# Kernel optimization log

Hardware: AMD Instinct MI355X
Metric: run time of the kernel (lower is better)

Reference implementation:

```python
import jax, jax.numpy as jnp
import numpy as np

S, L, B = 64, 64, 16
D_IN, D_ATTN = 1024, 512


def setup_inputs() -> dict:
    key = jax.random.key(0)
    ks = jax.random.split(key, 8)
    context = jax.random.normal(ks[0], (S, L, B, D_IN), dtype=jnp.float32)
    query = jax.random.normal(ks[1], (L, B, D_IN), dtype=jnp.float32)
    mask = jnp.ones((S, L, B), dtype=jnp.int32)
    # Linear params (torch layout: weight [out, in], bias [out])
    sc = 1.0 / np.sqrt(D_IN)
    Wc = jax.random.uniform(ks[2], (D_ATTN, D_IN), minval=-sc, maxval=sc, dtype=jnp.float32)
    bc = jax.random.uniform(ks[3], (D_ATTN,), minval=-sc, maxval=sc, dtype=jnp.float32)
    Wq = jax.random.uniform(ks[4], (D_ATTN, D_IN), minval=-sc, maxval=sc, dtype=jnp.float32)
    bq = jax.random.uniform(ks[5], (D_ATTN,), minval=-sc, maxval=sc, dtype=jnp.float32)
    v = jax.random.uniform(ks[6], (D_ATTN,), dtype=jnp.float32)  # torch.rand -> U[0,1)
    return {"context": context, "query": query, "mask": mask,
            "Wc": Wc, "bc": bc, "Wq": Wq, "bq": bq, "v": v}


def reference(context, query, mask, Wc, bc, Wq, bq, v):
    # context: [s,l,b,din], query: [l,b,din]
    context_proj = jnp.einsum('slbi,di->slbd', context, Wc) + bc  # [s,l,b,da]
    query_proj = jnp.einsum('lbi,di->lbd', query, Wq) + bq        # [l,b,da]
    scores = jnp.tanh(context_proj + query_proj[None])            # [s,l,b,da]
    scores = jnp.einsum('slbd,d->slb', scores, v)                 # [s,l,b]
    scores = jnp.where(mask == 0, jnp.float32(-1e9), scores)
    alpha = jax.nn.softmax(scores, axis=0)                        # softmax over s
    attn_output = jnp.einsum('slb,slbd->lbd', alpha, context)     # [l,b,din]
    return (attn_output, alpha)
```

## Files before the change

kernel.cpp:

```cpp
#include <hip/hip_runtime.h>
#include <hip/hip_fp16.h>
#include <stdint.h>

#define S_DIM 64
#define L_DIM 64
#define B_DIM 16
#define LB    1024
#define DIN   1024
#define DA    512
#define M_TOT 65536

using f16x8 = __attribute__((ext_vector_type(8))) _Float16;
using f32x4 = __attribute__((ext_vector_type(4))) float;

typedef const __attribute__((address_space(1))) void* gas_ptr;
typedef __attribute__((address_space(3))) void* las_ptr;

__device__ __forceinline__ void load_lds16(const void* g, void* l) {
    __builtin_amdgcn_global_load_lds((gas_ptr)g, (las_ptr)l, 16, 0, 0);
}

__device__ __forceinline__ float fast_tanh(float x) {
    return 1.0f - 2.0f / (__expf(2.0f * x) + 1.0f);
}

__global__ void cvt_all(const float* __restrict__ Wc, const float* __restrict__ Wq,
                        const float* __restrict__ q,
                        _Float16* __restrict__ Wch, _Float16* __restrict__ Wqh,
                        _Float16* __restrict__ Qh) {
    int i = blockIdx.x * 256 + threadIdx.x;
    if (i < DA * DIN)            Wch[i] = (_Float16)Wc[i];
    else if (i < 2 * DA * DIN)   Wqh[i - DA * DIN] = (_Float16)Wq[i - DA * DIN];
    else                         Qh[i - 2 * DA * DIN] = (_Float16)q[i - 2 * DA * DIN];
}

__global__ __launch_bounds__(256) void ctx_cvt(const float* __restrict__ src,
                                               _Float16* __restrict__ dst) {
    const size_t nchunk = (size_t)M_TOT * DIN / 8;
    size_t stride = (size_t)gridDim.x * 256;
    for (size_t c = (size_t)blockIdx.x * 256 + threadIdx.x; c < nchunk; c += stride) {
        f32x4 a = *(const f32x4*)(src + c * 8);
        f32x4 b = *(const f32x4*)(src + c * 8 + 4);
        f16x8 h = {(_Float16)a[0], (_Float16)a[1], (_Float16)a[2], (_Float16)a[3],
                   (_Float16)b[0], (_Float16)b[1], (_Float16)b[2], (_Float16)b[3]};
        *(f16x8*)(dst + c * 8) = h;
    }
}

__global__ __launch_bounds__(256) void qp_gemm(
    const _Float16* __restrict__ Qh,
    const _Float16* __restrict__ Wqh,
    const float* __restrict__ bq, const float* __restrict__ bc,
    float* __restrict__ qp)
{
    __shared__ __align__(16) _Float16 lA[64 * 64];
    __shared__ __align__(16) _Float16 lB[64 * 64];
    const int t = threadIdx.x;
    const int w = t >> 6, lane = t & 63;
    const int quad = lane >> 4, m16 = lane & 15;
    const int n0 = blockIdx.x * 64, lb0 = blockIdx.y * 64;

    f32x4 acc[4] = {};

    for (int kt = 0; kt < DIN / 64; ++kt) {
#pragma unroll
        for (int i = 0; i < 2; ++i) {
            int c = (w * 2 + i) * 64 + lane;
            int row = c >> 3;
            int kc = (c & 7) ^ (row & 7);
            load_lds16(Qh  + (size_t)(lb0 + row) * DIN + kt * 64 + kc * 8, (char*)lA + (size_t)c * 16);
            load_lds16(Wqh + (size_t)(n0  + row) * DIN + kt * 64 + kc * 8, (char*)lB + (size_t)c * 16);
        }
        __syncthreads();
#pragma unroll
        for (int kk = 0; kk < 64; kk += 32) {
            int cq = (kk >> 3) + quad;
            int ar = 16 * w + m16;
            f16x8 a = *(const f16x8*)((const char*)lA + ar * 128 + ((cq ^ (ar & 7)) * 16));
#pragma unroll
            for (int j = 0; j < 4; ++j) {
                int br = 16 * j + m16;
                f16x8 b = *(const f16x8*)((const char*)lB + br * 128 + ((cq ^ (br & 7)) * 16));
                acc[j] = __builtin_amdgcn_mfma_f32_16x16x32_f16(a, b, acc[j], 0, 0, 0);
            }
        }
        __syncthreads();
    }
#pragma unroll
    for (int j = 0; j < 4; ++j) {
        int n = n0 + 16 * j + m16;
        float bias = bq[n] + bc[n];
#pragma unroll
        for (int r = 0; r < 4; ++r) {
            int lb = lb0 + 16 * w + quad * 4 + r;
            qp[(size_t)lb * DA + n] = acc[j][r] + bias;
        }
    }
}

__global__ __launch_bounds__(256) void score_gemm2(
    const _Float16* __restrict__ ctxh,
    const _Float16* __restrict__ Wch,
    const float* __restrict__ qp,
    const float* __restrict__ v,
    float* __restrict__ scores)
{
    __shared__ __align__(16) _Float16 lA[128 * 64];
    __shared__ __align__(16) _Float16 lB[128 * 64];
    __shared__ float lP[2][128];

    const int t = threadIdx.x;
    const int w = t >> 6, lane = t & 63;
    const int quad = lane >> 4, m16 = lane & 15;
    const int wm = w & 1, wn = w >> 1;

    int bid = blockIdx.x;
    int xcd = bid & 7;
    int j2 = bid >> 3;
    int nq = j2 & 3;
    int mb = ((j2 >> 2) << 3) | xcd;
    const int m0 = mb * 128;
    const int n0 = nq * 128;

    f32x4 acc[4][4] = {};

    for (int kt = 0; kt < DIN / 64; ++kt) {
#pragma unroll
        for (int i = 0; i < 4; ++i) {
            int c = (w * 4 + i) * 64 + lane;
            int row = c >> 3;
            int kc = (c & 7) ^ (row & 7);
            load_lds16(ctxh + (size_t)(m0 + row) * DIN + kt * 64 + kc * 8,
                       (char*)lA + (size_t)c * 16);
            load_lds16(Wch  + (size_t)(n0 + row) * DIN + kt * 64 + kc * 8,
                       (char*)lB + (size_t)c * 16);
        }
        __syncthreads();
#pragma unroll
        for (int kk = 0; kk < 64; kk += 32) {
            int cq = (kk >> 3) + quad;
            f16x8 a[4], b[4];
#pragma unroll
            for (int i = 0; i < 4; ++i) {
                int ar = wm * 64 + 16 * i + m16;
                a[i] = *(const f16x8*)((const char*)lA + ar * 128 + ((cq ^ (ar & 7)) * 16));
            }
#pragma unroll
            for (int j = 0; j < 4; ++j) {
                int br = wn * 64 + 16 * j + m16;
                b[j] = *(const f16x8*)((const char*)lB + br * 128 + ((cq ^ (br & 7)) * 16));
            }
#pragma unroll
            for (int i = 0; i < 4; ++i)
#pragma unroll
                for (int j = 0; j < 4; ++j)
                    acc[i][j] = __builtin_amdgcn_mfma_f32_16x16x32_f16(a[i], b[j], acc[i][j], 0, 0, 0);
        }
        __syncthreads();
    }

    float vv[4];
    int nn[4];
#pragma unroll
    for (int j = 0; j < 4; ++j) { nn[j] = n0 + wn * 64 + 16 * j + m16; vv[j] = v[nn[j]]; }

    float part[16];
#pragma unroll
    for (int i = 0; i < 4; ++i) {
#pragma unroll
        for (int r = 0; r < 4; ++r) {
            int gm = m0 + wm * 64 + 16 * i + quad * 4 + r;
            int lb = gm & (LB - 1);
            float s = 0.f;
#pragma unroll
            for (int j = 0; j < 4; ++j) {
                float x = acc[i][j][r] + qp[(size_t)lb * DA + nn[j]];
                s += fast_tanh(x) * vv[j];
            }
            part[i * 4 + r] = s;
        }
    }
#pragma unroll
    for (int off = 1; off < 16; off <<= 1) {
#pragma unroll
        for (int k = 0; k < 16; ++k) part[k] += __shfl_xor(part[k], off, 64);
    }
    if (m16 == 0) {
#pragma unroll
        for (int k = 0; k < 16; ++k) {
            int row_local = wm * 64 + 16 * (k >> 2) + quad * 4 + (k & 3);
            lP[wn][row_local] = part[k];
        }
    }
    __syncthreads();
    if (t < 128) {
        float s = lP[0][t] + lP[1][t];
        atomicAdd(&scores[m0 + t], s);
    }
}

__global__ __launch_bounds__(256, 3) void score_gemm(
    const float* __restrict__ ctx, const _Float16* __restrict__ Wch,
    const float* __restrict__ qp, const float* __restrict__ v,
    float* __restrict__ scores)
{
    __shared__ __align__(16) _Float16 lA[128 * 64];
    __shared__ __align__(16) _Float16 lB[128 * 64];
    __shared__ float lP[2][128];

    const int t = threadIdx.x;
    const int w = t >> 6, lane = t & 63;
    const int quad = lane >> 4, m16 = lane & 15;
    const int wm = w & 1, wn = w >> 1;

    int bid = blockIdx.x;
    int xcd = bid & 7;
    int j2 = bid >> 3;
    int nq = j2 & 3;
    int mb = ((j2 >> 2) << 3) | xcd;
    const int m0 = mb * 128;
    const int n0 = nq * 128;

    f32x4 acc[4][4] = {};

    const int arow = t >> 1;
    const int akc4 = (t & 1) * 4;
    const float* gA = ctx + (size_t)(m0 + arow) * DIN + (t & 1) * 32;

    for (int kt = 0; kt < DIN / 64; ++kt) {
        {
            const float* p = gA + kt * 64;
            f32x4 f[8];
#pragma unroll
            for (int qd = 0; qd < 8; ++qd) f[qd] = *(const f32x4*)(p + qd * 4);
#pragma unroll
            for (int q2 = 0; q2 < 4; ++q2) {
                f16x8 h = {(_Float16)f[2*q2][0], (_Float16)f[2*q2][1],
                           (_Float16)f[2*q2][2], (_Float16)f[2*q2][3],
                           (_Float16)f[2*q2+1][0], (_Float16)f[2*q2+1][1],
                           (_Float16)f[2*q2+1][2], (_Float16)f[2*q2+1][3]};
                int c = akc4 + q2;
                *(f16x8*)((char*)lA + arow * 128 + ((c ^ (arow & 7)) * 16)) = h;
            }
        }
#pragma unroll
        for (int i = 0; i < 4; ++i) {
            int c = (w * 4 + i) * 64 + lane;
            int row = c >> 3;
            int kc = (c & 7) ^ (row & 7);
            load_lds16(Wch + (size_t)(n0 + row) * DIN + kt * 64 + kc * 8, (char*)lB + (size_t)c * 16);
        }
        __syncthreads();
#pragma unroll
        for (int kk = 0; kk < 64; kk += 32) {
            int cq = (kk >> 3) + quad;
            f16x8 a[4], b[4];
#pragma unroll
            for (int i = 0; i < 4; ++i) {
                int ar = wm * 64 + 16 * i + m16;
                a[i] = *(const f16x8*)((const char*)lA + ar * 128 + ((cq ^ (ar & 7)) * 16));
            }
#pragma unroll
            for (int j = 0; j < 4; ++j) {
                int br = wn * 64 + 16 * j + m16;
                b[j] = *(const f16x8*)((const char*)lB + br * 128 + ((cq ^ (br & 7)) * 16));
            }
#pragma unroll
            for (int i = 0; i < 4; ++i)
#pragma unroll
                for (int j = 0; j < 4; ++j)
                    acc[i][j] = __builtin_amdgcn_mfma_f32_16x16x32_f16(a[i], b[j], acc[i][j], 0, 0, 0);
        }
        __syncthreads();
    }

    float vv[4];
    int nn[4];
#pragma unroll
    for (int j = 0; j < 4; ++j) { nn[j] = n0 + wn * 64 + 16 * j + m16; vv[j] = v[nn[j]]; }

    float part[16];
#pragma unroll
    for (int i = 0; i < 4; ++i) {
#pragma unroll
        for (int r = 0; r < 4; ++r) {
            int gm = m0 + wm * 64 + 16 * i + quad * 4 + r;
            int lb = gm & (LB - 1);
            float s = 0.f;
#pragma unroll
            for (int j = 0; j < 4; ++j) {
                float x = acc[i][j][r] + qp[(size_t)lb * DA + nn[j]];
                s += fast_tanh(x) * vv[j];
            }
            part[i * 4 + r] = s;
        }
    }
#pragma unroll
    for (int off = 1; off < 16; off <<= 1) {
#pragma unroll
        for (int k = 0; k < 16; ++k) part[k] += __shfl_xor(part[k], off, 64);
    }
    if (m16 == 0) {
#pragma unroll
        for (int k = 0; k < 16; ++k) {
            int row_local = wm * 64 + 16 * (k >> 2) + quad * 4 + (k & 3);
            lP[wn][row_local] = part[k];
        }
    }
    __syncthreads();
    if (t < 128) {
        float s = lP[0][t] + lP[1][t];
        atomicAdd(&scores[m0 + t], s);
    }
}

__global__ __launch_bounds__(64) void softmax2(const float* __restrict__ scores,
                                               const int* __restrict__ mask,
                                               float* __restrict__ alpha) {
    int lb = blockIdx.x;
    int s = threadIdx.x;
    float x = scores[s * LB + lb];
    if (mask[s * LB + lb] == 0) x = -1e9f;
    float mx = x;
#pragma unroll
    for (int off = 1; off < 64; off <<= 1) mx = fmaxf(mx, __shfl_xor(mx, off, 64));
    float e = __expf(x - mx);
    float sum = e;
#pragma unroll
    for (int off = 1; off < 64; off <<= 1) sum += __shfl_xor(sum, off, 64);
    alpha[s * LB + lb] = e / sum;
}

__global__ __launch_bounds__(128) void weighted_sum2(
    const _Float16* __restrict__ ctxh, const float* __restrict__ alpha,
    float* __restrict__ out) {
    __shared__ float lAl[S_DIM];
    const int lb = blockIdx.x;
    const int t = threadIdx.x;
    if (t < S_DIM) lAl[t] = alpha[t * LB + lb];
    __syncthreads();
    float acc[8] = {};
    const _Float16* base = ctxh + (size_t)lb * DIN + t * 8;
#pragma unroll 4
    for (int s = 0; s < S_DIM; ++s) {
        float a = lAl[s];
        f16x8 c = *(const f16x8*)(base + (size_t)s * LB * DIN);
#pragma unroll
        for (int j = 0; j < 8; ++j) acc[j] += a * (float)c[j];
    }
    f32x4 lo = {acc[0], acc[1], acc[2], acc[3]};
    f32x4 hi = {acc[4], acc[5], acc[6], acc[7]};
    *(f32x4*)(out + (size_t)lb * DIN + t * 8) = lo;
    *(f32x4*)(out + (size_t)lb * DIN + t * 8 + 4) = hi;
}

__global__ __launch_bounds__(256) void weighted_sum(
    const float* __restrict__ ctx, const float* __restrict__ alpha,
    float* __restrict__ out) {
    __shared__ float lAl[S_DIM];
    const int lb = blockIdx.x;
    const int t = threadIdx.x;
    if (t < S_DIM) lAl[t] = alpha[t * LB + lb];
    __syncthreads();
    f32x4 acc = {0.f, 0.f, 0.f, 0.f};
    const float* base = ctx + (size_t)lb * DIN + t * 4;
#pragma unroll 4
    for (int s = 0; s < S_DIM; ++s) {
        float a = lAl[s];
        f32x4 c = *(const f32x4*)(base + (size_t)s * LB * DIN);
        acc += a * c;
    }
    *(f32x4*)(out + (size_t)lb * DIN + t * 4) = acc;
}

extern "C" void kernel_launch(void* const* d_in, const int* in_sizes, int n_in,
                              void* d_out, int out_size, void* d_ws, size_t ws_size,
                              hipStream_t stream) {
    (void)in_sizes; (void)n_in; (void)out_size;
    const float* ctx   = (const float*)d_in[0];
    const float* query = (const float*)d_in[1];
    const int*   mask  = (const int*)d_in[2];
    const float* Wc    = (const float*)d_in[3];
    const float* bc    = (const float*)d_in[4];
    const float* Wq    = (const float*)d_in[5];
    const float* bq    = (const float*)d_in[6];
    const float* v     = (const float*)d_in[7];

    float* out_attn  = (float*)d_out;
    float* out_alpha = (float*)d_out + (size_t)LB * DIN;

    char* ws = (char*)d_ws;
    _Float16* Wch = (_Float16*)(ws);
    _Float16* Wqh = (_Float16*)(ws + (1 << 20));
    _Float16* Qh  = (_Float16*)(ws + (2 << 20));
    float*    qp  = (float*)(ws + (4 << 20));
    float*    sc  = (float*)(ws + (6 << 20));
    _Float16* ctxh = (_Float16*)(ws + (8 << 20));

    const size_t need = (size_t)(8 + 128) << 20;
    const bool bigws = ws_size >= need;

    cvt_all<<<(2 * DA * DIN + LB * DIN) / 256, 256, 0, stream>>>(Wc, Wq, query, Wch, Wqh, Qh);
    hipMemsetAsync(sc, 0, (size_t)M_TOT * sizeof(float), stream);
    qp_gemm<<<dim3(DA / 64, LB / 64), 256, 0, stream>>>(Qh, Wqh, bq, bc, qp);

    if (bigws) {
        ctx_cvt<<<8192, 256, 0, stream>>>(ctx, ctxh);
        score_gemm2<<<2048, 256, 0, stream>>>(ctxh, Wch, qp, v, sc);
        softmax2<<<LB, 64, 0, stream>>>(sc, mask, out_alpha);
        weighted_sum2<<<LB, 128, 0, stream>>>(ctxh, out_alpha, out_attn);
    } else {
        score_gemm<<<2048, 256, 0, stream>>>(ctx, Wch, qp, v, sc);
        softmax2<<<LB, 64, 0, stream>>>(sc, mask, out_alpha);
        weighted_sum<<<LB, 256, 0, stream>>>(ctx, out_alpha, out_attn);
    }
}
```

Before: 540.1 us.

## Enlarge score GEMM tiles to 256x256 with double-buffered LDS and atomic-free partials

Replaces the 128x128 score GEMM with a 512-thread 256x256 tile kernel. It double-buffers LDS loads so the next K-slice is fetched during MFMA work, seeds the accumulators with the query projection, and uses setprio around the MFMA bursts. The two N-halves now write separate partial-score arrays, which the new softmax sums. That removes the memset and the global atomics. The trade is about 130KB of LDS per block, so only one block fits per CU, plus fewer blocks overall and more register pressure from 32 accumulator tiles.

New measurement: 541.7 us. About the same (+0.3%).

```diff
diff --git a/kernel.cpp b/kernel.cpp
--- a/kernel.cpp
+++ b/kernel.cpp
@@ -9,6 +9,11 @@
 #define DIN   1024
 #define DA    512
 #define M_TOT 65536
+
+#define BM 256
+#define BN 256
+#define BK 64
+#define NT (DIN / BK)
 
 using f16x8 = __attribute__((ext_vector_type(8))) _Float16;
 using f32x4 = __attribute__((ext_vector_type(4))) float;
@@ -98,16 +103,15 @@
     }
 }
 
-__global__ __launch_bounds__(256) void score_gemm2(
+__global__ __launch_bounds__(512, 2) void score_gemm3(
     const _Float16* __restrict__ ctxh,
     const _Float16* __restrict__ Wch,
     const float* __restrict__ qp,
     const float* __restrict__ v,
-    float* __restrict__ scores)
+    float* __restrict__ sc)
 {
-    __shared__ __align__(16) _Float16 lA[128 * 64];
-    __shared__ __align__(16) _Float16 lB[128 * 64];
-    __shared__ float lP[2][128];
+    __shared__ __align__(16) _Float16 lds[2][2][BM * BK];
+    __shared__ float lP[4][BM];
 
     const int t = threadIdx.x;
     const int w = t >> 6, lane = t & 63;
@@ -115,87 +119,122 @@
     const int wm = w & 1, wn = w >> 1;
 
     int bid = blockIdx.x;
-    int xcd = bid & 7;
-    int j2 = bid >> 3;
-    int nq = j2 & 3;
-    int mb = ((j2 >> 2) << 3) | xcd;
-    const int m0 = mb * 128;
-    const int n0 = nq * 128;
-
-    f32x4 acc[4][4] = {};
-
-    for (int kt = 0; kt < DIN / 64; ++kt) {
+    int swz = (bid & 7) * 64 + (bid >> 3);
+    const int nq = swz & 1;
+    const int mb = swz >> 1;
+    const int m0 = mb * BM;
+    const int n0 = nq * BN;
+    const int lb0 = m0 & (LB - 1);
+
+    auto stage = [&](int kt, int buf) {
 #pragma unroll
         for (int i = 0; i < 4; ++i) {
             int c = (w * 4 + i) * 64 + lane;
             int row = c >> 3;
             int kc = (c & 7) ^ (row & 7);
-            load_lds16(ctxh + (size_t)(m0 + row) * DIN + kt * 64 + kc * 8,
-                       (char*)lA + (size_t)c * 16);
-            load_lds16(Wch  + (size_t)(n0 + row) * DIN + kt * 64 + kc * 8,
-                       (char*)lB + (size_t)c * 16);
-        }
-        __syncthreads();
-#pragma unroll
-        for (int kk = 0; kk < 64; kk += 32) {
-            int cq = (kk >> 3) + quad;
-            f16x8 a[4], b[4];
-#pragma unroll
-            for (int i = 0; i < 4; ++i) {
-                int ar = wm * 64 + 16 * i + m16;
-                a[i] = *(const f16x8*)((const char*)lA + ar * 128 + ((cq ^ (ar & 7)) * 16));
-            }
+            load_lds16(ctxh + (size_t)(m0 + row) * DIN + kt * BK + kc * 8,
+                       (char*)lds[buf][0] + (size_t)c * 16);
+            load_lds16(Wch  + (size_t)(n0 + row) * DIN + kt * BK + kc * 8,
+                       (char*)lds[buf][1] + (size_t)c * 16);
+        }
+    };
+
+    stage(0, 0);
+
+    f32x4 acc[8][4];
+#pragma unroll
+    for (int i = 0; i < 8; ++i) {
+        int rl = wm * 128 + 16 * i + quad * 4;
+#pragma unroll
+        for (int j = 0; j < 4; ++j) {
+            int n = n0 + wn * 64 + 16 * j + m16;
+#pragma unroll
+            for (int r = 0; r < 4; ++r)
+                acc[i][j][r] = qp[(size_t)(lb0 + rl + r) * DA + n];
+        }
+    }
+
+    asm volatile("s_waitcnt vmcnt(0)" ::: "memory");
+    __builtin_amdgcn_s_barrier();
+    __builtin_amdgcn_sched_barrier(0);
+
+    for (int kt = 0; kt < NT; ++kt) {
+        const int cur = kt & 1;
+        if (kt + 1 < NT) stage(kt + 1, cur ^ 1);
+        const _Float16* lA = lds[cur][0];
+        const _Float16* lB = lds[cur][1];
+
+        f16x8 b[2][4];
+#pragma unroll
+        for (int kk = 0; kk < 2; ++kk)
 #pragma unroll
             for (int j = 0; j < 4; ++j) {
                 int br = wn * 64 + 16 * j + m16;
-                b[j] = *(const f16x8*)((const char*)lB + br * 128 + ((cq ^ (br & 7)) * 16));
-            }
-#pragma unroll
-            for (int i = 0; i < 4; ++i)
+                int cq = kk * 4 + quad;
+                b[kk][j] = *(const f16x8*)((const char*)lB + br * 128 + ((cq ^ (br & 7)) * 16));
+            }
+
+#pragma unroll
+        for (int p = 0; p < 4; ++p) {
+            f16x8 a[2][2];
+#pragma unroll
+            for (int ii = 0; ii < 2; ++ii) {
+                int ar = wm * 128 + 16 * (2 * p + ii) + m16;
+#pragma unroll
+                for (int kk = 0; kk < 2; ++kk) {
+                    int cq = kk * 4 + quad;
+                    a[ii][kk] = *(const f16x8*)((const char*)lA + ar * 128 + ((cq ^ (ar & 7)) * 16));
+                }
+            }
+            __builtin_amdgcn_s_barrier();
+            __builtin_amdgcn_s_setprio(1);
+#pragma unroll
+            for (int ii = 0; ii < 2; ++ii)
 #pragma unroll
                 for (int j = 0; j < 4; ++j)
-                    acc[i][j] = __builtin_amdgcn_mfma_f32_16x16x32_f16(a[i], b[j], acc[i][j], 0, 0, 0);
-        }
-        __syncthreads();
+#pragma unroll
+                    for (int kk = 0; kk < 2; ++kk)
+                        acc[2 * p + ii][j] = __builtin_amdgcn_mfma_f32_16x16x32_f16(
+                            a[ii][kk], b[kk][j], acc[2 * p + ii][j], 0, 0, 0);
+            __builtin_amdgcn_s_setprio(0);
+        }
+
+        asm volatile("s_waitcnt vmcnt(0)" ::: "memory");
+        __builtin_amdgcn_s_barrier();
+        __builtin_amdgcn_sched_barrier(0);
     }
 
     float vv[4];
-    int nn[4];
-#pragma unroll
-    for (int j = 0; j < 4; ++j) { nn[j] = n0 + wn * 64 + 16 * j + m16; vv[j] = v[nn[j]]; }
-
-    float part[16];
-#pragma unroll
-    for (int i = 0; i < 4; ++i) {
+#pragma unroll
+    for (int j = 0; j < 4; ++j) vv[j] = v[n0 + wn * 64 + 16 * j + m16];
+
+    float part[32];
+#pragma unroll
+    for (int i = 0; i < 8; ++i)
 #pragma unroll
         for (int r = 0; r < 4; ++r) {
-            int gm = m0 + wm * 64 + 16 * i + quad * 4 + r;
-            int lb = gm & (LB - 1);
             float s = 0.f;
 #pragma unroll
-            for (int j = 0; j < 4; ++j) {
-                float x = acc[i][j][r] + qp[(size_t)lb * DA + nn[j]];
-                s += fast_tanh(x) * vv[j];
-            }
+            for (int j = 0; j < 4; ++j)
+                s += fast_tanh(acc[i][j][r]) * vv[j];
             part[i * 4 + r] = s;
         }
-    }
 #pragma unroll
     for (int off = 1; off < 16; off <<= 1) {
 #pragma unroll
-        for (int k = 0; k < 16; ++k) part[k] += __shfl_xor(part[k], off, 64);
+        for (int k = 0; k < 32; ++k) part[k] += __shfl_xor(part[k], off, 64);
     }
     if (m16 == 0) {
 #pragma unroll
-        for (int k = 0; k < 16; ++k) {
-            int row_local = wm * 64 + 16 * (k >> 2) + quad * 4 + (k & 3);
-            lP[wn][row_local] = part[k];
+        for (int k = 0; k < 32; ++k) {
+            int rl = wm * 128 + 16 * (k >> 2) + quad * 4 + (k & 3);
+            lP[wn][rl] = part[k];
         }
     }
     __syncthreads();
-    if (t < 128) {
-        float s = lP[0][t] + lP[1][t];
-        atomicAdd(&scores[m0 + t], s);
+    if (t < BM) {
+        float s = lP[0][t] + lP[1][t] + lP[2][t] + lP[3][t];
+        sc[(size_t)nq * M_TOT + m0 + t] = s;
     }
 }
 
@@ -216,10 +255,10 @@
     int bid = blockIdx.x;
     int xcd = bid & 7;
     int j2 = bid >> 3;
-    int nq = j2 & 3;
-    int mb = ((j2 >> 2) << 3) | xcd;
-    const int m0 = mb * 128;
-    const int n0 = nq * 128;
+    int nqf = j2 & 3;
+    int mbf = ((j2 >> 2) << 3) | xcd;
+    const int m0 = mbf * 128;
+    const int n0 = nqf * 128;
 
     f32x4 acc[4][4] = {};
 
@@ -312,6 +351,24 @@
         float s = lP[0][t] + lP[1][t];
         atomicAdd(&scores[m0 + t], s);
     }
+}
+
+__global__ __launch_bounds__(64) void softmax3(const float* __restrict__ sc,
+                                               const int* __restrict__ mask,
+                                               float* __restrict__ alpha) {
+    int lb = blockIdx.x;
+    int s = threadIdx.x;
+    int m = s * LB + lb;
+    float x = sc[m] + sc[M_TOT + m];
+    if (mask[m] == 0) x = -1e9f;
+    float mx = x;
+#pragma unroll
+    for (int off = 1; off < 64; off <<= 1) mx = fmaxf(mx, __shfl_xor(mx, off, 64));
+    float e = __expf(x - mx);
+    float sum = e;
+#pragma unroll
+    for (int off = 1; off < 64; off <<= 1) sum += __shfl_xor(sum, off, 64);
+    alpha[m] = e / sum;
 }
 
 __global__ __launch_bounds__(64) void softmax2(const float* __restrict__ scores,
@@ -341,7 +398,7 @@
     __syncthreads();
     float acc[8] = {};
     const _Float16* base = ctxh + (size_t)lb * DIN + t * 8;
-#pragma unroll 4
+#pragma unroll 8
     for (int s = 0; s < S_DIM; ++s) {
         float a = lAl[s];
         f16x8 c = *(const f16x8*)(base + (size_t)s * LB * DIN);
@@ -401,15 +458,15 @@
     const bool bigws = ws_size >= need;
 
     cvt_all<<<(2 * DA * DIN + LB * DIN) / 256, 256, 0, stream>>>(Wc, Wq, query, Wch, Wqh, Qh);
-    hipMemsetAsync(sc, 0, (size_t)M_TOT * sizeof(float), stream);
     qp_gemm<<<dim3(DA / 64, LB / 64), 256, 0, stream>>>(Qh, Wqh, bq, bc, qp);
 
     if (bigws) {
         ctx_cvt<<<8192, 256, 0, stream>>>(ctx, ctxh);
-        score_gemm2<<<2048, 256, 0, stream>>>(ctxh, Wch, qp, v, sc);
-        softmax2<<<LB, 64, 0, stream>>>(sc, mask, out_alpha);
+        score_gemm3<<<(M_TOT / BM) * (DA / BN), 512, 0, stream>>>(ctxh, Wch, qp, v, sc);
+        softmax3<<<LB, 64, 0, stream>>>(sc, mask, out_alpha);
         weighted_sum2<<<LB, 128, 0, stream>>>(ctxh, out_alpha, out_attn);
     } else {
+        hipMemsetAsync(sc, 0, (size_t)M_TOT * sizeof(float), stream);
         score_gemm<<<2048, 256, 0, stream>>>(ctx, Wch, qp, v, sc);
         softmax2<<<LB, 64, 0, stream>>>(sc, mask, out_alpha);
         weighted_sum<<<LB, 256, 0, stream>>>(ctx, out_alpha, out_attn);
```

## Fuse context fp16 conversion into full-width score GEMM with double-buffered weights

Applied to the files above, without the earlier changes.

Removes the separate ctx_cvt pass. The score kernel now reads fp32 context directly, converts it to fp16 in registers, writes it to LDS and also stores the fp16 copy for the later weighted sum. Each block covers all 512 attention columns, so scores are written directly instead of through atomics, and the memset is dropped. Accumulators start from the query projection, the Wc tile is double-buffered in LDS, and the fp32 A tile is prefetched one step ahead. In exchange Wc is re-read by every M block, the 512-thread blocks carry large accumulators (register pressure), and the fp16 context is still written once.

Result: faster. 483.4 us (-10.5%).

```diff
diff --git a/kernel.cpp b/kernel.cpp
--- a/kernel.cpp
+++ b/kernel.cpp
@@ -9,6 +9,11 @@
 #define DIN   1024
 #define DA    512
 #define M_TOT 65536
+
+#define BM 128
+#define BN 512
+#define BK 64
+#define NT (DIN / BK)
 
 using f16x8 = __attribute__((ext_vector_type(8))) _Float16;
 using f32x4 = __attribute__((ext_vector_type(4))) float;
@@ -32,19 +37,6 @@
     if (i < DA * DIN)            Wch[i] = (_Float16)Wc[i];
     else if (i < 2 * DA * DIN)   Wqh[i - DA * DIN] = (_Float16)Wq[i - DA * DIN];
     else                         Qh[i - 2 * DA * DIN] = (_Float16)q[i - 2 * DA * DIN];
-}
-
-__global__ __launch_bounds__(256) void ctx_cvt(const float* __restrict__ src,
-                                               _Float16* __restrict__ dst) {
-    const size_t nchunk = (size_t)M_TOT * DIN / 8;
-    size_t stride = (size_t)gridDim.x * 256;
-    for (size_t c = (size_t)blockIdx.x * 256 + threadIdx.x; c < nchunk; c += stride) {
-        f32x4 a = *(const f32x4*)(src + c * 8);
-        f32x4 b = *(const f32x4*)(src + c * 8 + 4);
-        f16x8 h = {(_Float16)a[0], (_Float16)a[1], (_Float16)a[2], (_Float16)a[3],
-                   (_Float16)b[0], (_Float16)b[1], (_Float16)b[2], (_Float16)b[3]};
-        *(f16x8*)(dst + c * 8) = h;
-    }
 }
 
 __global__ __launch_bounds__(256) void qp_gemm(
@@ -98,16 +90,17 @@
     }
 }
 
-__global__ __launch_bounds__(256) void score_gemm2(
-    const _Float16* __restrict__ ctxh,
+__global__ __launch_bounds__(512, 2) void score_gemm4(
+    const float* __restrict__ ctx,
     const _Float16* __restrict__ Wch,
     const float* __restrict__ qp,
     const float* __restrict__ v,
-    float* __restrict__ scores)
+    _Float16* __restrict__ ctxh,
+    float* __restrict__ sc)
 {
-    __shared__ __align__(16) _Float16 lA[128 * 64];
-    __shared__ __align__(16) _Float16 lB[128 * 64];
-    __shared__ float lP[2][128];
+    __shared__ __align__(16) _Float16 lA[BM * BK];
+    __shared__ __align__(16) _Float16 lB[2][BN * BK];
+    __shared__ float lP[4][BM];
 
     const int t = threadIdx.x;
     const int w = t >> 6, lane = t & 63;
@@ -115,71 +108,115 @@
     const int wm = w & 1, wn = w >> 1;
 
     int bid = blockIdx.x;
-    int xcd = bid & 7;
-    int j2 = bid >> 3;
-    int nq = j2 & 3;
-    int mb = ((j2 >> 2) << 3) | xcd;
-    const int m0 = mb * 128;
-    const int n0 = nq * 128;
-
-    f32x4 acc[4][4] = {};
-
-    for (int kt = 0; kt < DIN / 64; ++kt) {
-#pragma unroll
-        for (int i = 0; i < 4; ++i) {
-            int c = (w * 4 + i) * 64 + lane;
+    int mb = (bid & 7) * 64 + (bid >> 3);
+    const int m0 = mb * BM;
+    const int lb0 = m0 & (LB - 1);
+
+    const int arow = t >> 2;
+    const int c0   = (t & 3) * 2;
+
+    auto stageB = [&](int kt, int buf) {
+#pragma unroll
+        for (int i = 0; i < 8; ++i) {
+            int c = (w * 8 + i) * 64 + lane;
             int row = c >> 3;
             int kc = (c & 7) ^ (row & 7);
-            load_lds16(ctxh + (size_t)(m0 + row) * DIN + kt * 64 + kc * 8,
-                       (char*)lA + (size_t)c * 16);
-            load_lds16(Wch  + (size_t)(n0 + row) * DIN + kt * 64 + kc * 8,
-                       (char*)lB + (size_t)c * 16);
-        }
-        __syncthreads();
-#pragma unroll
-        for (int kk = 0; kk < 64; kk += 32) {
-            int cq = (kk >> 3) + quad;
-            f16x8 a[4], b[4];
+            load_lds16(Wch + (size_t)row * DIN + kt * BK + kc * 8,
+                       (char*)lB[buf] + (size_t)c * 16);
+        }
+    };
+
+    f32x4 pf[4];
+    auto issueA = [&](int kt) {
+        const float* p = ctx + (size_t)(m0 + arow) * DIN + kt * BK + c0 * 8;
+        pf[0] = *(const f32x4*)(p);
+        pf[1] = *(const f32x4*)(p + 4);
+        pf[2] = *(const f32x4*)(p + 8);
+        pf[3] = *(const f32x4*)(p + 12);
+    };
+
+    stageB(0, 0);
+    issueA(0);
+
+    f32x4 acc[4][8];
+#pragma unroll
+    for (int i = 0; i < 4; ++i) {
+        int rl = lb0 + wm * 64 + 16 * i + quad * 4;
+#pragma unroll
+        for (int j = 0; j < 8; ++j) {
+            int n = wn * 128 + 16 * j + m16;
+#pragma unroll
+            for (int r = 0; r < 4; ++r)
+                acc[i][j][r] = qp[(size_t)(rl + r) * DA + n];
+        }
+    }
+
+    asm volatile("s_waitcnt vmcnt(0)" ::: "memory");
+    __builtin_amdgcn_s_barrier();
+    __builtin_amdgcn_sched_barrier(0);
+
+    for (int kt = 0; kt < NT; ++kt) {
+        const int cur = kt & 1;
+
+        f16x8 h0 = {(_Float16)pf[0][0], (_Float16)pf[0][1], (_Float16)pf[0][2], (_Float16)pf[0][3],
+                    (_Float16)pf[1][0], (_Float16)pf[1][1], (_Float16)pf[1][2], (_Float16)pf[1][3]};
+        f16x8 h1 = {(_Float16)pf[2][0], (_Float16)pf[2][1], (_Float16)pf[2][2], (_Float16)pf[2][3],
+                    (_Float16)pf[3][0], (_Float16)pf[3][1], (_Float16)pf[3][2], (_Float16)pf[3][3]};
+        *(f16x8*)((char*)lA + arow * 128 + (((c0)     ^ (arow & 7)) * 16)) = h0;
+        *(f16x8*)((char*)lA + arow * 128 + (((c0 + 1) ^ (arow & 7)) * 16)) = h1;
+        _Float16* cd = ctxh + (size_t)(m0 + arow) * DIN + kt * BK + c0 * 8;
+        *(f16x8*)cd = h0;
+        *(f16x8*)(cd + 8) = h1;
+
+        if (kt + 1 < NT) { stageB(kt + 1, cur ^ 1); issueA(kt + 1); }
+
+        asm volatile("s_waitcnt lgkmcnt(0)" ::: "memory");
+        __builtin_amdgcn_s_barrier();
+        __builtin_amdgcn_sched_barrier(0);
+
+#pragma unroll
+        for (int kk2 = 0; kk2 < 2; ++kk2) {
+            int cq = kk2 * 4 + quad;
+            f16x8 a[4], b[8];
 #pragma unroll
             for (int i = 0; i < 4; ++i) {
                 int ar = wm * 64 + 16 * i + m16;
                 a[i] = *(const f16x8*)((const char*)lA + ar * 128 + ((cq ^ (ar & 7)) * 16));
             }
 #pragma unroll
-            for (int j = 0; j < 4; ++j) {
-                int br = wn * 64 + 16 * j + m16;
-                b[j] = *(const f16x8*)((const char*)lB + br * 128 + ((cq ^ (br & 7)) * 16));
-            }
+            for (int j = 0; j < 8; ++j) {
+                int br = wn * 128 + 16 * j + m16;
+                b[j] = *(const f16x8*)((const char*)lB[cur] + br * 128 + ((cq ^ (br & 7)) * 16));
+            }
+            __builtin_amdgcn_s_setprio(1);
 #pragma unroll
             for (int i = 0; i < 4; ++i)
 #pragma unroll
-                for (int j = 0; j < 4; ++j)
+                for (int j = 0; j < 8; ++j)
                     acc[i][j] = __builtin_amdgcn_mfma_f32_16x16x32_f16(a[i], b[j], acc[i][j], 0, 0, 0);
-        }
-        __syncthreads();
-    }
-
-    float vv[4];
-    int nn[4];
-#pragma unroll
-    for (int j = 0; j < 4; ++j) { nn[j] = n0 + wn * 64 + 16 * j + m16; vv[j] = v[nn[j]]; }
+            __builtin_amdgcn_s_setprio(0);
+        }
+
+        asm volatile("s_waitcnt vmcnt(0)" ::: "memory");
+        __builtin_amdgcn_s_barrier();
+        __builtin_amdgcn_sched_barrier(0);
+    }
+
+    float vv[8];
+#pragma unroll
+    for (int j = 0; j < 8; ++j) vv[j] = v[wn * 128 + 16 * j + m16];
 
     float part[16];
 #pragma unroll
-    for (int i = 0; i < 4; ++i) {
+    for (int i = 0; i < 4; ++i)
 #pragma unroll
         for (int r = 0; r < 4; ++r) {
-            int gm = m0 + wm * 64 + 16 * i + quad * 4 + r;
-            int lb = gm & (LB - 1);
             float s = 0.f;
 #pragma unroll
-            for (int j = 0; j < 4; ++j) {
-                float x = acc[i][j][r] + qp[(size_t)lb * DA + nn[j]];
-                s += fast_tanh(x) * vv[j];
-            }
+            for (int j = 0; j < 8; ++j)
+                s += fast_tanh(acc[i][j][r]) * vv[j];
             part[i * 4 + r] = s;
         }
-    }
 #pragma unroll
     for (int off = 1; off < 16; off <<= 1) {
 #pragma unroll
@@ -188,14 +225,14 @@
     if (m16 == 0) {
 #pragma unroll
         for (int k = 0; k < 16; ++k) {
-            int row_local = wm * 64 + 16 * (k >> 2) + quad * 4 + (k & 3);
-            lP[wn][row_local] = part[k];
+            int rl = wm * 64 + 16 * (k >> 2) + quad * 4 + (k & 3);
+            lP[wn][rl] = part[k];
         }
     }
     __syncthreads();
-    if (t < 128) {
-        float s = lP[0][t] + lP[1][t];
-        atomicAdd(&scores[m0 + t], s);
+    if (t < BM) {
+        float s = lP[0][t] + lP[1][t] + lP[2][t] + lP[3][t];
+        sc[m0 + t] = s;
     }
 }
 
@@ -216,10 +253,10 @@
     int bid = blockIdx.x;
     int xcd = bid & 7;
     int j2 = bid >> 3;
-    int nq = j2 & 3;
-    int mb = ((j2 >> 2) << 3) | xcd;
-    const int m0 = mb * 128;
-    const int n0 = nq * 128;
+    int nqf = j2 & 3;
+    int mbf = ((j2 >> 2) << 3) | xcd;
+    const int m0 = mbf * 128;
+    const int n0 = nqf * 128;
 
     f32x4 acc[4][4] = {};
 
@@ -341,7 +378,7 @@
     __syncthreads();
     float acc[8] = {};
     const _Float16* base = ctxh + (size_t)lb * DIN + t * 8;
-#pragma unroll 4
+#pragma unroll 8
     for (int s = 0; s < S_DIM; ++s) {
         float a = lAl[s];
         f16x8 c = *(const f16x8*)(base + (size_t)s * LB * DIN);
@@ -401,15 +438,14 @@
     const bool bigws = ws_size >= need;
 
     cvt_all<<<(2 * DA * DIN + LB * DIN) / 256, 256, 0, stream>>>(Wc, Wq, query, Wch, Wqh, Qh);
-    hipMemsetAsync(sc, 0, (size_t)M_TOT * sizeof(float), stream);
     qp_gemm<<<dim3(DA / 64, LB / 64), 256, 0, stream>>>(Qh, Wqh, bq, bc, qp);
 
     if (bigws) {
-        ctx_cvt<<<8192, 256, 0, stream>>>(ctx, ctxh);
-        score_gemm2<<<2048, 256, 0, stream>>>(ctxh, Wch, qp, v, sc);
+        score_gemm4<<<M_TOT / BM, 512, 0, stream>>>(ctx, Wch, qp, v, ctxh, sc);
         softmax2<<<LB, 64, 0, stream>>>(sc, mask, out_alpha);
         weighted_sum2<<<LB, 128, 0, stream>>>(ctxh, out_alpha, out_attn);
     } else {
+        hipMemsetAsync(sc, 0, (size_t)M_TOT * sizeof(float), stream);
         score_gemm<<<2048, 256, 0, stream>>>(ctx, Wch, qp, v, sc);
         softmax2<<<LB, 64, 0, stream>>>(sc, mask, out_alpha);
         weighted_sum<<<LB, 256, 0, stream>>>(ctx, out_alpha, out_attn);
```
